# Kernel tuning notes

Measured on AMD Instinct MI355X. Metric: run time of the kernel, lower is better.

## Reference

```python
import jax, jax.numpy as jnp
import numpy as np

B, M, N, D = 1, 128, 256, 256   # batch, msa rows, residues, node dim
DE = 128                        # edge (pair) dim
H, DH = 8, 64                   # heads, dim_head
INNER = H * DH


def setup_inputs() -> dict:
    key = jax.random.key(0)
    ks = jax.random.split(key, 10)
    s = 0.02
    return {
        "x": jax.random.normal(ks[0], (B, M, N, D), jnp.float32),
        "edges": jax.random.normal(ks[1], (B, N, N, DE), jnp.float32),
        "mask": jnp.ones((B, M, N), dtype=bool),
        "ln_g": jnp.ones((D,), jnp.float32),
        "ln_b": jnp.zeros((D,), jnp.float32),
        "Wq": jax.random.normal(ks[2], (D, INNER), jnp.float32) * s,
        "Wkv": jax.random.normal(ks[3], (D, 2 * INNER), jnp.float32) * s,
        "Wg": jax.random.normal(ks[4], (D, INNER), jnp.float32) * s,
        "bg": jnp.ones((INNER,), jnp.float32),
        "Wo": jax.random.normal(ks[5], (INNER, D), jnp.float32) * s,
        "bo": jnp.zeros((D,), jnp.float32),
        "Wb": jax.random.normal(ks[6], (DE, H), jnp.float32) * s,
    }


def reference(x, edges, mask, ln_g, ln_b, Wq, Wkv, Wg, bg, Wo, bo, Wb):
    b, m, n, d = x.shape
    scale = DH ** -0.5
    # LayerNorm over node dim (biased variance, eps=1e-5 as torch default)
    mu = x.mean(-1, keepdims=True)
    var = x.var(-1, keepdims=True)
    xn = (x - mu) / jnp.sqrt(var + 1e-5) * ln_g + ln_b

    # pair bias: [b, h, i, j], shared across MSA rows
    bias = jnp.einsum('bijc,ch->bhij', edges, Wb)

    # projections, split heads: [b, m, n, h, dh]
    q = jnp.einsum('bmnd,de->bmne', xn, Wq).reshape(b, m, n, H, DH) * scale
    kv = jnp.einsum('bmnd,de->bmne', xn, Wkv)
    k = kv[..., :INNER].reshape(b, m, n, H, DH)
    v = kv[..., INNER:].reshape(b, m, n, H, DH)

    # tied queries: mean over MSA rows (global_query_attn, tie_dim=m)
    qm = q.mean(axis=1)  # [b, n, h, dh]
    dots = jnp.einsum('bihd,bmjhd->bmhij', qm, k) + bias[:, None]  # [b,m,h,i,j]

    pair_mask = mask[:, :, None, :, None] & mask[:, :, None, None, :]
    neg = -jnp.finfo(dots.dtype).max
    dots = jnp.where(pair_mask, dots, neg)
    attn = jax.nn.softmax(dots, axis=-1)

    out = jnp.einsum('bmhij,bmjhd->bmihd', attn, v).reshape(b, m, n, INNER)
    gates = jax.nn.sigmoid(jnp.einsum('bmnd,de->bmne', xn, Wg) + bg)
    out = out * gates
    return jnp.einsum('bmne,ed->bmnd', out, Wo) + bo
```

## Files before the change

### kernel.cpp

```cpp
#include <hip/hip_runtime.h>
#include <stdint.h>


#define DEV __device__ __forceinline__

typedef __attribute__((ext_vector_type(8))) short bf16x8;
typedef __attribute__((ext_vector_type(4))) float f32x4;

DEV short f2bf(float f) {
  union { float f; uint32_t u; } v; v.f = f;
  uint32_t r = v.u + 0x7fffu + ((v.u >> 16) & 1u);
  return (short)(r >> 16);
}
DEV float bf2f(short s) {
  union { uint32_t u; float f; } v; v.u = ((uint32_t)(uint16_t)s) << 16;
  return v.f;
}

#define GLDS16(gp, lp) __builtin_amdgcn_global_load_lds( \
    (__attribute__((address_space(1))) void*)(gp),       \
    (__attribute__((address_space(3))) void*)(lp), 16, 0, 0)

__global__ __launch_bounds__(256) void k_ln(const float* __restrict__ x,
                                            const float* __restrict__ g,
                                            const float* __restrict__ b,
                                            short* __restrict__ xn) {
  int wave = threadIdx.x >> 6, lane = threadIdx.x & 63;
  long row = (long)blockIdx.x * 4 + wave;
  const float* xr = x + row * 256;
  float4 v = ((const float4*)xr)[lane];
  float s = v.x + v.y + v.z + v.w;
  float sq = v.x*v.x + v.y*v.y + v.z*v.z + v.w*v.w;
#pragma unroll
  for (int o = 1; o < 64; o <<= 1) { s += __shfl_xor(s, o); sq += __shfl_xor(sq, o); }
  float mu = s * (1.f/256.f);
  float var = sq * (1.f/256.f) - mu*mu;
  float rstd = rsqrtf(var + 1e-5f);
  float4 gg = ((const float4*)g)[lane];
  float4 bb = ((const float4*)b)[lane];
  short4 o4;
  o4.x = f2bf((v.x-mu)*rstd*gg.x + bb.x);
  o4.y = f2bf((v.y-mu)*rstd*gg.y + bb.y);
  o4.z = f2bf((v.z-mu)*rstd*gg.z + bb.z);
  o4.w = f2bf((v.w-mu)*rstd*gg.w + bb.w);
  ((short4*)(xn + row * 256))[lane] = o4;
}

__global__ __launch_bounds__(256) void k_wt(const float* __restrict__ Wq,
                                            const float* __restrict__ Wkv,
                                            const float* __restrict__ Wg,
                                            const float* __restrict__ Wo,
                                            short* __restrict__ WT,
                                            short* __restrict__ WoT) {
  int idx = blockIdx.x * 256 + threadIdx.x;
  if (idx < 2048 * 256) {
    int n = idx >> 8, k = idx & 255;
    float v;
    if (n < 512)       v = Wq[k * 512 + n];
    else if (n < 1536) v = Wkv[k * 1024 + (n - 512)];
    else               v = Wg[k * 512 + (n - 1536)];
    WT[idx] = f2bf(v);
  } else {
    int j = idx - 2048 * 256;
    int k = j & 511;
    WoT[j] = f2bf(Wo[k * 256 + (j >> 9)]);
  }
}

__global__ __launch_bounds__(256) void k_bias(const float* __restrict__ edges,
                                              const float* __restrict__ Wb,
                                              float* __restrict__ biasF) {
  int pair = blockIdx.x * 4 + (threadIdx.x >> 6);
  int lane = threadIdx.x & 63;
  const float* e = edges + (long)pair * 128;
  float a0 = e[lane], a1 = e[lane + 64];
  float acc[8];
#pragma unroll
  for (int h = 0; h < 8; ++h)
    acc[h] = a0 * Wb[lane * 8 + h] + a1 * Wb[(lane + 64) * 8 + h];
#pragma unroll
  for (int o = 1; o < 64; o <<= 1) {
#pragma unroll
    for (int h = 0; h < 8; ++h) acc[h] += __shfl_xor(acc[h], o);
  }
  if (lane == 0) {
    int i = pair >> 8, j = pair & 255;
    long base = ((long)(i >> 4) * 16 + (j >> 4)) * 256 +
                (((i >> 2) & 3) * 16 + (j & 15)) * 4 + (i & 3);
#pragma unroll
    for (int h = 0; h < 8; ++h) biasF[(long)h * 65536 + base] = acc[h];
  }
}

__global__ __launch_bounds__(256) void k_xbar(const short* __restrict__ xn,
                                              float* __restrict__ xbar) {
  int i = blockIdx.x, d = threadIdx.x;
  const short* p = xn + (long)i * 256 + d;
  float s = 0.f;
#pragma unroll 4
  for (int mm = 0; mm < 128; ++mm) s += bf2f(p[(long)mm * 65536]);
  xbar[i * 256 + d] = s * (1.f / 128.f);
}

__global__ __launch_bounds__(256) void k_qmg(const float* __restrict__ xbar,
                                             const short* __restrict__ WT,
                                             short* __restrict__ qm) {
  int i = blockIdx.x;
  int e0 = threadIdx.x;
  const float* xb = xbar + i * 256;
  float acc0 = 0.f, acc1 = 0.f;
  for (int d = 0; d < 256; d += 8) {
    bf16x8 w0 = *(const bf16x8*)&WT[e0 * 256 + d];
    bf16x8 w1 = *(const bf16x8*)&WT[(e0 + 256) * 256 + d];
#pragma unroll
    for (int t = 0; t < 8; ++t) {
      float xv = xb[d + t];
      acc0 += xv * bf2f(w0[t]);
      acc1 += xv * bf2f(w1[t]);
    }
  }
  qm[((e0 >> 6) * 256 + i) * 64 + (e0 & 63)] = f2bf(acc0 * 0.125f);
  int e1 = e0 + 256;
  qm[((e1 >> 6) * 256 + i) * 64 + (e1 & 63)] = f2bf(acc1 * 0.125f);
}

__global__ __launch_bounds__(256, 3) void k_proj(const short* __restrict__ A,
                                                 const short* __restrict__ B,
                                                 short* __restrict__ kRM,
                                                 short* __restrict__ vT,
                                                 short* __restrict__ gRM,
                                                 const float* __restrict__ bg) {
  __shared__ short As[2][128 * 32];
  __shared__ short Bs[2][128 * 32];
  int tid = threadIdx.x;
  int wave = tid >> 6, lane = tid & 63;
  int quad = lane >> 4, l15 = lane & 15;
  long row0 = (long)blockIdx.y * 128;
  int col0 = 512 + blockIdx.x * 128;
  int wi = (wave >> 1) * 64, wj = (wave & 1) * 64;
  f32x4 acc[4][4] = {};
  const short* Ab = A + row0 * 256;
  const short* Bb = B + (long)col0 * 256;
  int r0 = tid >> 2, gc0 = tid & 3;
  int g0 = (gc0 ^ ((r0 >> 1) & 3)) * 8;
  int g1 = (gc0 ^ (((r0 + 64) >> 1) & 3)) * 8;

#define PSTAGE(buf, k0) do {                                          \
    GLDS16(Ab + (long)r0 * 256 + (k0) + g0,        &As[buf][tid * 8]);          \
    GLDS16(Ab + (long)(r0 + 64) * 256 + (k0) + g1, &As[buf][(tid + 256) * 8]);  \
    GLDS16(Bb + (long)r0 * 256 + (k0) + g0,        &Bs[buf][tid * 8]);          \
    GLDS16(Bb + (long)(r0 + 64) * 256 + (k0) + g1, &Bs[buf][(tid + 256) * 8]);  \
  } while (0)

  PSTAGE(0, 0);
  for (int it = 0; it < 8; ++it) {
    int cur = it & 1;
    __syncthreads();
    if (it < 7) PSTAGE(1 - cur, (it + 1) * 32);
    bf16x8 a[4], b[4];
#pragma unroll
    for (int t = 0; t < 4; ++t) {
      int ra = wi + t * 16 + l15;
      int rb = wj + t * 16 + l15;
      a[t] = *(const bf16x8*)&As[cur][ra * 32 + ((quad ^ ((ra >> 1) & 3)) * 8)];
      b[t] = *(const bf16x8*)&Bs[cur][rb * 32 + ((quad ^ ((rb >> 1) & 3)) * 8)];
    }
#pragma unroll
    for (int ti = 0; ti < 4; ++ti)
#pragma unroll
      for (int tj = 0; tj < 4; ++tj)
        acc[ti][tj] = __builtin_amdgcn_mfma_f32_16x16x32_bf16(a[ti], b[tj], acc[ti][tj], 0, 0, 0);
  }
#undef PSTAGE

  int rg = col0 >> 9;
#pragma unroll
  for (int ti = 0; ti < 4; ++ti)
#pragma unroll
    for (int tj = 0; tj < 4; ++tj) {
      int gcol = col0 + wj + tj * 16 + l15;
      long grow = row0 + wi + ti * 16 + quad * 4;
      if (rg == 3) {
#pragma unroll
        for (int r = 0; r < 4; ++r) {
          float v = 1.f / (1.f + __expf(-(acc[ti][tj][r] + bg[gcol - 1536])));
          gRM[(grow + r) * 512 + (gcol - 1536)] = f2bf(v);
        }
      } else if (rg == 1) {
#pragma unroll
        for (int r = 0; r < 4; ++r)
          kRM[(grow + r) * 512 + (gcol - 512)] = f2bf(acc[ti][tj][r]);
      } else {
        short4 pk;
        pk.x = f2bf(acc[ti][tj][0]); pk.y = f2bf(acc[ti][tj][1]);
        pk.z = f2bf(acc[ti][tj][2]); pk.w = f2bf(acc[ti][tj][3]);
        *(short4*)&vT[(long)(gcol - 1024) * 32768 + grow] = pk;
      }
    }
}

__global__ __launch_bounds__(512, 4) void k_attn(const short* __restrict__ qm,
                                                 const short* __restrict__ kRM,
                                                 const short* __restrict__ vT,
                                                 const short* __restrict__ gRM,
                                                 const float* __restrict__ biasF,
                                                 short* __restrict__ outA) {
  __shared__ short kL[256 * 64];
  __shared__ short vL[64 * 256];
  __shared__ short pL[8 * 16 * 64];
  int m = blockIdx.x, h = blockIdx.y;
  int tid = threadIdx.x;
  int wave = tid >> 6, lane = tid & 63;
  int quad = lane >> 4, l15 = lane & 15;
  int l7 = l15 & 7;

  const short* kg_ = kRM + ((long)m * 256) * 512 + h * 64;
  const short* vg_ = vT + (long)(h * 64) * 32768 + m * 256;
#pragma unroll
  for (int it = 0; it < 4; ++it) {
    int slot = it * 512 + tid;
    int row = slot >> 3;
    int g = (slot & 7) ^ (row & 7);
    GLDS16(kg_ + (long)row * 512 + g * 8, &kL[slot * 8]);
    int d = slot >> 5;
    int jg = (slot & 31) ^ (d & 7);
    GLDS16(vg_ + (long)d * 32768 + jg * 8, &vL[slot * 8]);
  }

  const short* qmh = qm + h * (256 * 64);
  bf16x8 aq[2][2];
#pragma unroll
  for (int ti = 0; ti < 2; ++ti)
#pragma unroll
    for (int ks = 0; ks < 2; ++ks)
      aq[ti][ks] = *(const bf16x8*)&qmh[(wave * 32 + ti * 16 + l15) * 64 + ks * 32 + quad * 8];

  f32x4 o[2][4] = {};
  float lrow[2][4] = {};
  const float* bF = biasF + ((long)h * 16 + wave * 2) * 16 * 256 + lane * 4;

  __syncthreads();

  for (int jc = 0; jc < 4; ++jc) {
    f32x4 s[2][4];
#pragma unroll
    for (int ti = 0; ti < 2; ++ti)
#pragma unroll
      for (int tj = 0; tj < 4; ++tj)
        s[ti][tj] = *(const f32x4*)&bF[((long)ti * 16 + jc * 4 + tj) * 256];
#pragma unroll
    for (int tj = 0; tj < 4; ++tj) {
      int jrow = jc * 64 + tj * 16 + l15;
      bf16x8 b0 = *(const bf16x8*)&kL[jrow * 64 + ((quad ^ l7) * 8)];
      bf16x8 b1 = *(const bf16x8*)&kL[jrow * 64 + (((4 + quad) ^ l7) * 8)];
#pragma unroll
      for (int ti = 0; ti < 2; ++ti) {
        s[ti][tj] = __builtin_amdgcn_mfma_f32_16x16x32_bf16(aq[ti][0], b0, s[ti][tj], 0, 0, 0);
        s[ti][tj] = __builtin_amdgcn_mfma_f32_16x16x32_bf16(aq[ti][1], b1, s[ti][tj], 0, 0, 0);
      }
    }

#pragma unroll
    for (int ti = 0; ti < 2; ++ti) {
#pragma unroll
      for (int r = 0; r < 4; ++r) {
        int rloc = quad * 4 + r;
#pragma unroll
        for (int tj = 0; tj < 4; ++tj) {
          float p = __expf(s[ti][tj][r]);
          lrow[ti][r] += p;
          int col = tj * 16 + l15;
          int slot = (col >> 3) ^ (rloc & 7);
          pL[wave * 1024 + rloc * 64 + slot * 8 + (col & 7)] = f2bf(p);
        }
      }
      bf16x8 ap0 = *(const bf16x8*)&pL[wave * 1024 + l15 * 64 + ((quad ^ l7) * 8)];
      bf16x8 ap1 = *(const bf16x8*)&pL[wave * 1024 + l15 * 64 + (((4 + quad) ^ l7) * 8)];
#pragma unroll
      for (int td = 0; td < 4; ++td) {
        int drow = td * 16 + l15;
        bf16x8 bv0 = *(const bf16x8*)&vL[drow * 256 + (jc * 8 + (quad ^ l7)) * 8];
        bf16x8 bv1 = *(const bf16x8*)&vL[drow * 256 + (jc * 8 + ((4 + quad) ^ l7)) * 8];
        o[ti][td] = __builtin_amdgcn_mfma_f32_16x16x32_bf16(ap0, bv0, o[ti][td], 0, 0, 0);
        o[ti][td] = __builtin_amdgcn_mfma_f32_16x16x32_bf16(ap1, bv1, o[ti][td], 0, 0, 0);
      }
    }
  }

#pragma unroll
  for (int ti = 0; ti < 2; ++ti)
#pragma unroll
    for (int r = 0; r < 4; ++r) {
      float l = lrow[ti][r];
#pragma unroll
      for (int off = 1; off < 16; off <<= 1) l += __shfl_xor(l, off);
      float inv = 1.f / l;
      int i = wave * 32 + ti * 16 + quad * 4 + r;
      long rowoff = (long)m * 256 + i;
#pragma unroll
      for (int td = 0; td < 4; ++td) {
        int dh = td * 16 + l15;
        float gv = bf2f(gRM[rowoff * 512 + h * 64 + dh]);
        outA[rowoff * 512 + h * 64 + dh] = f2bf(o[ti][td][r] * inv * gv);
      }
    }
}

__global__ __launch_bounds__(256, 3) void k_out(const short* __restrict__ A,
                                                const short* __restrict__ B,
                                                float* __restrict__ out,
                                                const float* __restrict__ bo) {
  __shared__ short As[2][128 * 32];
  __shared__ short Bs[2][128 * 32];
  int tid = threadIdx.x;
  int wave = tid >> 6, lane = tid & 63;
  int quad = lane >> 4, l15 = lane & 15;
  long row0 = (long)blockIdx.y * 128;
  int col0 = blockIdx.x * 128;
  int wi = (wave >> 1) * 64, wj = (wave & 1) * 64;
  f32x4 acc[4][4] = {};
  const short* Ab = A + row0 * 512;
  const short* Bb = B + (long)col0 * 512;
  int r0 = tid >> 2, gc0 = tid & 3;
  int g0 = (gc0 ^ ((r0 >> 1) & 3)) * 8;
  int g1 = (gc0 ^ (((r0 + 64) >> 1) & 3)) * 8;

#define OSTAGE(buf, k0) do {                                          \
    GLDS16(Ab + (long)r0 * 512 + (k0) + g0,        &As[buf][tid * 8]);          \
    GLDS16(Ab + (long)(r0 + 64) * 512 + (k0) + g1, &As[buf][(tid + 256) * 8]);  \
    GLDS16(Bb + (long)r0 * 512 + (k0) + g0,        &Bs[buf][tid * 8]);          \
    GLDS16(Bb + (long)(r0 + 64) * 512 + (k0) + g1, &Bs[buf][(tid + 256) * 8]);  \
  } while (0)

  OSTAGE(0, 0);
  for (int it = 0; it < 16; ++it) {
    int cur = it & 1;
    __syncthreads();
    if (it < 15) OSTAGE(1 - cur, (it + 1) * 32);
    bf16x8 a[4], b[4];
#pragma unroll
    for (int t = 0; t < 4; ++t) {
      int ra = wi + t * 16 + l15;
      int rb = wj + t * 16 + l15;
      a[t] = *(const bf16x8*)&As[cur][ra * 32 + ((quad ^ ((ra >> 1) & 3)) * 8)];
      b[t] = *(const bf16x8*)&Bs[cur][rb * 32 + ((quad ^ ((rb >> 1) & 3)) * 8)];
    }
#pragma unroll
    for (int ti = 0; ti < 4; ++ti)
#pragma unroll
      for (int tj = 0; tj < 4; ++tj)
        acc[ti][tj] = __builtin_amdgcn_mfma_f32_16x16x32_bf16(a[ti], b[tj], acc[ti][tj], 0, 0, 0);
  }
#undef OSTAGE

#pragma unroll
  for (int ti = 0; ti < 4; ++ti)
#pragma unroll
    for (int tj = 0; tj < 4; ++tj)
#pragma unroll
      for (int r = 0; r < 4; ++r) {
        long grow = row0 + wi + ti * 16 + quad * 4 + r;
        int gcol = col0 + wj + tj * 16 + l15;
        out[grow * 256 + gcol] = acc[ti][tj][r] + bo[gcol];
      }
}

extern "C" void kernel_launch(void* const* d_in, const int* in_sizes, int n_in,
                              void* d_out, int out_size, void* d_ws, size_t ws_size,
                              hipStream_t stream) {
  (void)in_sizes; (void)n_in; (void)out_size; (void)ws_size;
  const float* x     = (const float*)d_in[0];
  const float* edges = (const float*)d_in[1];
  const float* ln_g  = (const float*)d_in[3];
  const float* ln_b  = (const float*)d_in[4];
  const float* Wq    = (const float*)d_in[5];
  const float* Wkv   = (const float*)d_in[6];
  const float* Wg    = (const float*)d_in[7];
  const float* bg    = (const float*)d_in[8];
  const float* Wo    = (const float*)d_in[9];
  const float* bo    = (const float*)d_in[10];
  const float* Wb    = (const float*)d_in[11];
  float* out = (float*)d_out;

  char* ws = (char*)d_ws;
  short* xn    = (short*)ws;  ws += 32768L * 256 * 2;
  short* WT    = (short*)ws;  ws += 2048L * 256 * 2;
  short* WoT   = (short*)ws;  ws += 256L * 512 * 2;
  short* kRM   = (short*)ws;  ws += 32768L * 512 * 2;
  short* vT    = (short*)ws;  ws += 512L * 32768 * 2;
  short* gRM   = (short*)ws;  ws += 32768L * 512 * 2;
  float* biasF = (float*)ws;  ws += 8L * 256 * 256 * 4;
  float* xbar  = (float*)ws;  ws += 256L * 256 * 4;
  short* qmb   = (short*)ws;  ws += 8L * 256 * 64 * 2;
  short* outA  = (short*)ws;  ws += 32768L * 512 * 2;

  k_ln<<<8192, 256, 0, stream>>>(x, ln_g, ln_b, xn);
  k_wt<<<2560, 256, 0, stream>>>(Wq, Wkv, Wg, Wo, WT, WoT);
  k_bias<<<16384, 256, 0, stream>>>(edges, Wb, biasF);
  k_xbar<<<256, 256, 0, stream>>>(xn, xbar);
  k_qmg<<<256, 256, 0, stream>>>(xbar, WT, qmb);
  k_proj<<<dim3(12, 256), 256, 0, stream>>>(xn, WT, kRM, vT, gRM, bg);
  k_attn<<<dim3(128, 8), 512, 0, stream>>>(qmb, kRM, vT, gRM, biasF, outA);
  k_out<<<dim3(2, 256), 256, 0, stream>>>(outA, WoT, out, bo);
}
```

Baseline: 294.9 us.

## Load weight tiles to registers and stage projection epilogue through LDS

In k_proj and k_out the B (weight) operand is now loaded straight from global memory into registers, prefetched one step ahead, instead of being staged through LDS. This shrinks LDS use and the ds_read traffic. k_proj's epilogue now writes its results into a padded LDS tile and then issues coalesced 16-byte global stores for k, g and the transposed v, replacing scattered 2-byte and 8-byte stores. k_out's tile is halved to 64 rows with double the grid and occupancy hint raised to 4, trading per-block reuse for more blocks in flight and more register-held B loads that may hit cache less.

```diff
diff --git a/kernel.cpp b/kernel.cpp
--- a/kernel.cpp
+++ b/kernel.cpp
@@ -130,8 +130,7 @@
                                                  short* __restrict__ vT,
                                                  short* __restrict__ gRM,
                                                  const float* __restrict__ bg) {
-  __shared__ short As[2][128 * 32];
-  __shared__ short Bs[2][128 * 32];
+  __shared__ short SM[18432];
   int tid = threadIdx.x;
   int wave = tid >> 6, lane = tid & 63;
   int quad = lane >> 4, l15 = lane & 15;
@@ -145,58 +144,87 @@
   int g0 = (gc0 ^ ((r0 >> 1) & 3)) * 8;
   int g1 = (gc0 ^ (((r0 + 64) >> 1) & 3)) * 8;
 
-#define PSTAGE(buf, k0) do {                                          \
-    GLDS16(Ab + (long)r0 * 256 + (k0) + g0,        &As[buf][tid * 8]);          \
-    GLDS16(Ab + (long)(r0 + 64) * 256 + (k0) + g1, &As[buf][(tid + 256) * 8]);  \
-    GLDS16(Bb + (long)r0 * 256 + (k0) + g0,        &Bs[buf][tid * 8]);          \
-    GLDS16(Bb + (long)(r0 + 64) * 256 + (k0) + g1, &Bs[buf][(tid + 256) * 8]);  \
+#define PSTAGE(buf, k0) do {                                                        \
+    GLDS16(Ab + (long)r0 * 256 + (k0) + g0,        &SM[(buf) * 4096 + tid * 8]);    \
+    GLDS16(Ab + (long)(r0 + 64) * 256 + (k0) + g1, &SM[(buf) * 4096 + (tid + 256) * 8]); \
   } while (0)
-
+#define BLOAD(dst, k0) do {                                                         \
+    _Pragma("unroll")                                                               \
+    for (int tj = 0; tj < 4; ++tj)                                                  \
+      dst[tj] = *(const bf16x8*)&Bb[(long)(wj + tj * 16 + l15) * 256 + (k0) + quad * 8]; \
+  } while (0)
+
+  bf16x8 bn[4], bc[4];
   PSTAGE(0, 0);
+  BLOAD(bn, 0);
   for (int it = 0; it < 8; ++it) {
     int cur = it & 1;
     __syncthreads();
     if (it < 7) PSTAGE(1 - cur, (it + 1) * 32);
-    bf16x8 a[4], b[4];
+#pragma unroll
+    for (int tj = 0; tj < 4; ++tj) bc[tj] = bn[tj];
+    if (it < 7) BLOAD(bn, (it + 1) * 32);
+    bf16x8 a[4];
 #pragma unroll
     for (int t = 0; t < 4; ++t) {
       int ra = wi + t * 16 + l15;
-      int rb = wj + t * 16 + l15;
-      a[t] = *(const bf16x8*)&As[cur][ra * 32 + ((quad ^ ((ra >> 1) & 3)) * 8)];
-      b[t] = *(const bf16x8*)&Bs[cur][rb * 32 + ((quad ^ ((rb >> 1) & 3)) * 8)];
+      a[t] = *(const bf16x8*)&SM[cur * 4096 + ra * 32 + ((quad ^ ((ra >> 1) & 3)) * 8)];
     }
 #pragma unroll
     for (int ti = 0; ti < 4; ++ti)
 #pragma unroll
       for (int tj = 0; tj < 4; ++tj)
-        acc[ti][tj] = __builtin_amdgcn_mfma_f32_16x16x32_bf16(a[ti], b[tj], acc[ti][tj], 0, 0, 0);
+        acc[ti][tj] = __builtin_amdgcn_mfma_f32_16x16x32_bf16(a[ti], bc[tj], acc[ti][tj], 0, 0, 0);
   }
 #undef PSTAGE
+#undef BLOAD
 
   int rg = col0 >> 9;
-#pragma unroll
-  for (int ti = 0; ti < 4; ++ti)
-#pragma unroll
-    for (int tj = 0; tj < 4; ++tj) {
-      int gcol = col0 + wj + tj * 16 + l15;
-      long grow = row0 + wi + ti * 16 + quad * 4;
-      if (rg == 3) {
+  __syncthreads();
+  if (rg != 2) {
+#pragma unroll
+    for (int ti = 0; ti < 4; ++ti)
+#pragma unroll
+      for (int tj = 0; tj < 4; ++tj) {
+        int lc = wj + tj * 16 + l15;
 #pragma unroll
         for (int r = 0; r < 4; ++r) {
-          float v = 1.f / (1.f + __expf(-(acc[ti][tj][r] + bg[gcol - 1536])));
-          gRM[(grow + r) * 512 + (gcol - 1536)] = f2bf(v);
+          int lr = wi + ti * 16 + quad * 4 + r;
+          float v = acc[ti][tj][r];
+          if (rg == 3) v = 1.f / (1.f + __expf(-(v + bg[col0 - 1536 + lc])));
+          SM[lr * 144 + lc] = f2bf(v);
         }
-      } else if (rg == 1) {
-#pragma unroll
-        for (int r = 0; r < 4; ++r)
-          kRM[(grow + r) * 512 + (gcol - 512)] = f2bf(acc[ti][tj][r]);
-      } else {
+      }
+    __syncthreads();
+    short* dst = (rg == 1) ? kRM : gRM;
+    int colbase = col0 - ((rg == 1) ? 512 : 1536);
+    int rr = tid >> 1, cc = (tid & 1) * 64;
+#pragma unroll
+    for (int c8 = 0; c8 < 8; ++c8) {
+      bf16x8 vv = *(const bf16x8*)&SM[rr * 144 + cc + c8 * 8];
+      *(bf16x8*)&dst[(row0 + rr) * 512 + colbase + cc + c8 * 8] = vv;
+    }
+  } else {
+#pragma unroll
+    for (int ti = 0; ti < 4; ++ti)
+#pragma unroll
+      for (int tj = 0; tj < 4; ++tj) {
+        int lc = wj + tj * 16 + l15;
+        int lr = wi + ti * 16 + quad * 4;
         short4 pk;
         pk.x = f2bf(acc[ti][tj][0]); pk.y = f2bf(acc[ti][tj][1]);
         pk.z = f2bf(acc[ti][tj][2]); pk.w = f2bf(acc[ti][tj][3]);
-        *(short4*)&vT[(long)(gcol - 1024) * 32768 + grow] = pk;
-      }
-    }
+        *(short4*)&SM[lc * 136 + lr] = pk;
+      }
+    __syncthreads();
+    int cc = tid >> 1, rh = (tid & 1) * 64;
+    long dbase = (long)(col0 - 1024 + cc) * 32768 + row0 + rh;
+#pragma unroll
+    for (int j8 = 0; j8 < 8; ++j8) {
+      bf16x8 vv = *(const bf16x8*)&SM[cc * 136 + rh + j8 * 8];
+      *(bf16x8*)&vT[dbase + j8 * 8] = vv;
+    }
+  }
 }
 
 __global__ __launch_bounds__(512, 4) void k_attn(const short* __restrict__ qm,
@@ -306,55 +334,57 @@
     }
 }
 
-__global__ __launch_bounds__(256, 3) void k_out(const short* __restrict__ A,
+__global__ __launch_bounds__(256, 4) void k_out(const short* __restrict__ A,
                                                 const short* __restrict__ B,
                                                 float* __restrict__ out,
                                                 const float* __restrict__ bo) {
-  __shared__ short As[2][128 * 32];
-  __shared__ short Bs[2][128 * 32];
+  __shared__ short As[2][64 * 32];
   int tid = threadIdx.x;
   int wave = tid >> 6, lane = tid & 63;
   int quad = lane >> 4, l15 = lane & 15;
-  long row0 = (long)blockIdx.y * 128;
+  long row0 = (long)blockIdx.y * 64;
   int col0 = blockIdx.x * 128;
-  int wi = (wave >> 1) * 64, wj = (wave & 1) * 64;
-  f32x4 acc[4][4] = {};
+  int wi = (wave >> 1) * 32, wj = (wave & 1) * 64;
+  f32x4 acc[2][4] = {};
   const short* Ab = A + row0 * 512;
   const short* Bb = B + (long)col0 * 512;
   int r0 = tid >> 2, gc0 = tid & 3;
   int g0 = (gc0 ^ ((r0 >> 1) & 3)) * 8;
-  int g1 = (gc0 ^ (((r0 + 64) >> 1) & 3)) * 8;
-
-#define OSTAGE(buf, k0) do {                                          \
-    GLDS16(Ab + (long)r0 * 512 + (k0) + g0,        &As[buf][tid * 8]);          \
-    GLDS16(Ab + (long)(r0 + 64) * 512 + (k0) + g1, &As[buf][(tid + 256) * 8]);  \
-    GLDS16(Bb + (long)r0 * 512 + (k0) + g0,        &Bs[buf][tid * 8]);          \
-    GLDS16(Bb + (long)(r0 + 64) * 512 + (k0) + g1, &Bs[buf][(tid + 256) * 8]);  \
+
+#define OSTAGE(buf, k0) GLDS16(Ab + (long)r0 * 512 + (k0) + g0, &As[buf][tid * 8])
+#define OBLOAD(dst, k0) do {                                                        \
+    _Pragma("unroll")                                                               \
+    for (int tj = 0; tj < 4; ++tj)                                                  \
+      dst[tj] = *(const bf16x8*)&Bb[(long)(wj + tj * 16 + l15) * 512 + (k0) + quad * 8]; \
   } while (0)
 
+  bf16x8 bn[4], bc[4];
   OSTAGE(0, 0);
+  OBLOAD(bn, 0);
   for (int it = 0; it < 16; ++it) {
     int cur = it & 1;
     __syncthreads();
     if (it < 15) OSTAGE(1 - cur, (it + 1) * 32);
-    bf16x8 a[4], b[4];
-#pragma unroll
-    for (int t = 0; t < 4; ++t) {
+#pragma unroll
+    for (int tj = 0; tj < 4; ++tj) bc[tj] = bn[tj];
+    if (it < 15) OBLOAD(bn, (it + 1) * 32);
+    bf16x8 a[2];
+#pragma unroll
+    for (int t = 0; t < 2; ++t) {
       int ra = wi + t * 16 + l15;
-      int rb = wj + t * 16 + l15;
       a[t] = *(const bf16x8*)&As[cur][ra * 32 + ((quad ^ ((ra >> 1) & 3)) * 8)];
-      b[t] = *(const bf16x8*)&Bs[cur][rb * 32 + ((quad ^ ((rb >> 1) & 3)) * 8)];
-    }
-#pragma unroll
-    for (int ti = 0; ti < 4; ++ti)
+    }
+#pragma unroll
+    for (int ti = 0; ti < 2; ++ti)
 #pragma unroll
       for (int tj = 0; tj < 4; ++tj)
-        acc[ti][tj] = __builtin_amdgcn_mfma_f32_16x16x32_bf16(a[ti], b[tj], acc[ti][tj], 0, 0, 0);
+        acc[ti][tj] = __builtin_amdgcn_mfma_f32_16x16x32_bf16(a[ti], bc[tj], acc[ti][tj], 0, 0, 0);
   }
 #undef OSTAGE
-
-#pragma unroll
-  for (int ti = 0; ti < 4; ++ti)
+#undef OBLOAD
+
+#pragma unroll
+  for (int ti = 0; ti < 2; ++ti)
 #pragma unroll
     for (int tj = 0; tj < 4; ++tj)
 #pragma unroll
@@ -401,5 +431,5 @@
   k_qmg<<<256, 256, 0, stream>>>(xbar, WT, qmb);
   k_proj<<<dim3(12, 256), 256, 0, stream>>>(xn, WT, kRM, vT, gRM, bg);
   k_attn<<<dim3(128, 8), 512, 0, stream>>>(qmb, kRM, vT, gRM, biasF, outA);
-  k_out<<<dim3(2, 256), 256, 0, stream>>>(outA, WoT, out, bo);
-}
+  k_out<<<dim3(2, 512), 256, 0, stream>>>(outA, WoT, out, bo);
+}
```

New measurement: 345.6 us. 17.2% more time.
